# Optimization experiments

Hardware: AMD Instinct MI355X
Metric: run time of the kernel (lower is better)

The kernel has to match this reference:

```python
import jax, jax.numpy as jnp
import numpy as np
from jax import lax

RADIUS = 5


def setup_inputs() -> dict:
    key = jax.random.key(0)
    k1, k2 = jax.random.split(key)
    B, K, H, W = 4, 6, 128, 128
    win = 2 * RADIUS + 1
    labels = jax.random.uniform(k1, (B, K, H, W), dtype=jnp.float32)
    weights = jax.random.uniform(k2, (B, H * W, win, win), dtype=jnp.float32)
    return {"labels": labels, "weights": weights}


def reference(labels, weights):
    # labels:  [B, K, H, W]  class probabilities
    B, K, H, W = labels.shape
    win = 2 * RADIUS + 1
    N = H * W

    # Extract 11x11 patches around every pixel for all classes at once.
    patches = lax.conv_general_dilated_patches(
        labels, (win, win), (1, 1), padding=[(RADIUS, RADIUS), (RADIUS, RADIUS)]
    )
    patches = patches.reshape(B, K, win * win, N)

    w = weights.reshape(B, N, win * win)

    # sum over window of weights * P, per class: wp[b,k,n] = sum_o w[b,n,o] * patches[b,k,o,n]
    wp = jnp.einsum('bkon,bno->bkn', patches, w)

    p = labels.reshape(B, K, N)
    num = jnp.einsum('bkn,bkn->bk', p, wp)          # association
    den = jnp.einsum('bkn,bn->bk', p, w.sum(-1))    # degree
    L = num / den                                    # [B, K]

    # nn.L1Loss()(L, zeros) per class = mean_b |L[b,k]|
    losses = jnp.mean(jnp.abs(L), axis=0)            # [K]
    return K - jnp.sum(losses)
```

## Files before the change

### kernel.cpp

```cpp
#include <hip/hip_runtime.h>

#define RADIUS 5
#define WIN    11
#define WIN2   121
#define KCLS   6
#define HH     128
#define WW     128
#define BB     4
#define NPIX   (HH*WW)
#define TPB    128
#define PXB    32
#define NBLK   (BB*HH*(WW/PXB))
#define LABW   (PXB + 2*RADIUS)
#define NSITE  (WIN*LABW)
#define PLSTR  (NSITE*2)

__global__ __launch_bounds__(TPB, 4) void ncut_main(
    const float* __restrict__ labels,
    const float* __restrict__ weights,
    float* __restrict__ part) {
  __shared__ float shl[3 * PLSTR];
  __shared__ float shred[2 * 12];

  const int tid = threadIdx.x;
  const int blk = blockIdx.x;
  const int b   = blk >> 9;
  const int rem = blk & 511;
  const int y0  = rem >> 2;
  const int x0  = (rem & 3) * PXB;

  const float* labB = labels + (size_t)b * KCLS * NPIX;
  for (int s = tid; s < NSITE; s += TPB) {
    const int tr = s / LABW;
    const int tc = s - tr * LABW;
    const int gy = y0 - RADIUS + tr;
    const int gx = x0 + tc - RADIUS;
    const bool ok = ((unsigned)gy < (unsigned)HH) & ((unsigned)gx < (unsigned)WW);
    const float* lp = labB + (size_t)gy * WW + gx;
#pragma unroll
    for (int p = 0; p < 3; ++p) {
      float2 v = make_float2(0.f, 0.f);
      if (ok) {
        v.x = lp[(size_t)(2 * p) * NPIX];
        v.y = lp[(size_t)(2 * p + 1) * NPIX];
      }
      *reinterpret_cast<float2*>(shl + p * PLSTR + 2 * s) = v;
    }
  }
  __syncthreads();

  const int px = tid >> 2;
  const int q  = tid & 3;
  const size_t pxg = (size_t)b * NPIX + (size_t)y0 * WW + x0 + px;
  const int S  = (int)(pxg & 3);
  const float* wal = weights + pxg * WIN2 - S;
  const int T0 = 4 * q - S;

  float2 a0 = make_float2(0.f, 0.f);
  float2 a1 = make_float2(0.f, 0.f);
  float2 a2 = make_float2(0.f, 0.f);
  float wsum = 0.f;

#pragma unroll
  for (int g = 0; g < 8; ++g) {
    const int kq = (g == 7) ? ((q == 3) ? 30 : 28 + q) : 4 * g + q;
    const float4 wv = *reinterpret_cast<const float4*>(wal + 4 * kq);
#pragma unroll
    for (int m = 0; m < 4; ++m) {
      float w = (m == 0) ? wv.x : (m == 1) ? wv.y : (m == 2) ? wv.z : wv.w;
      int   t = 16 * g + m + T0;
      bool valid = true;
      if (g == 0) valid = (q != 0) | (m >= S);
      if (g == 7) valid = (q < 2) | ((q == 2) & (m <= S));
      if (!valid) { w = 0.0f; t = 0; }
      const int r  = (t * 5958) >> 16;
      const int li = px + t + (LABW - WIN) * r;
      const float2 v0 = *reinterpret_cast<const float2*>(shl + 2 * li);
      const float2 v1 = *reinterpret_cast<const float2*>(shl + PLSTR + 2 * li);
      const float2 v2 = *reinterpret_cast<const float2*>(shl + 2 * PLSTR + 2 * li);
      wsum += w;
      a0.x += w * v0.x; a0.y += w * v0.y;
      a1.x += w * v1.x; a1.y += w * v1.y;
      a2.x += w * v2.x; a2.y += w * v2.y;
    }
  }

#pragma unroll
  for (int off = 1; off <= 2; off <<= 1) {
    wsum += __shfl_xor(wsum, off);
    a0.x += __shfl_xor(a0.x, off); a0.y += __shfl_xor(a0.y, off);
    a1.x += __shfl_xor(a1.x, off); a1.y += __shfl_xor(a1.y, off);
    a2.x += __shfl_xor(a2.x, off); a2.y += __shfl_xor(a2.y, off);
  }

  const int lc = px + 5 * LABW + 5;
  const float2 c0 = *reinterpret_cast<const float2*>(shl + 2 * lc);
  const float2 c1 = *reinterpret_cast<const float2*>(shl + PLSTR + 2 * lc);
  const float2 c2 = *reinterpret_cast<const float2*>(shl + 2 * PLSTR + 2 * lc);
  float nv[KCLS] = {c0.x * a0.x, c0.y * a0.y, c1.x * a1.x,
                    c1.y * a1.y, c2.x * a2.x, c2.y * a2.y};
  float dv[KCLS] = {c0.x * wsum, c0.y * wsum, c1.x * wsum,
                    c1.y * wsum, c2.x * wsum, c2.y * wsum};

#pragma unroll
  for (int off = 4; off <= 32; off <<= 1) {
#pragma unroll
    for (int k = 0; k < KCLS; ++k) {
      nv[k] += __shfl_xor(nv[k], off);
      dv[k] += __shfl_xor(dv[k], off);
    }
  }
  const int wave = tid >> 6;
  if ((tid & 63) == 0) {
#pragma unroll
    for (int k = 0; k < KCLS; ++k) {
      shred[wave * 12 + k]     = nv[k];
      shred[wave * 12 + 6 + k] = dv[k];
    }
  }
  __syncthreads();
  if (tid < 12) {
    part[tid * NBLK + blk] = shred[tid] + shred[12 + tid];
  }
}

__global__ __launch_bounds__(256) void ncut_final(
    const float* __restrict__ part, float* __restrict__ out) {
  __shared__ float shf[4 * 48];
  const int t     = threadIdx.x;
  const int sumid = t >> 2;
  const int seg   = t & 3;
  if (sumid < 48) {
    const int isden = sumid / 24;
    const int bk    = sumid - isden * 24;
    const int b     = bk / KCLS;
    const int k     = bk - b * KCLS;
    const int slot  = isden * KCLS + k;
    const float* p  = part + (size_t)slot * NBLK + b * (NBLK / BB) + seg * 128;
    float s = 0.f;
#pragma unroll 8
    for (int i = 0; i < 32; ++i) {
      const float4 v = *reinterpret_cast<const float4*>(p + 4 * i);
      s += v.x + v.y + v.z + v.w;
    }
    shf[seg * 48 + sumid] = s;
  }
  __syncthreads();
  float val = 0.f;
  if (t < 24) {
    float num = 0.f, den = 0.f;
#pragma unroll
    for (int sg = 0; sg < 4; ++sg) {
      num += shf[sg * 48 + t];
      den += shf[sg * 48 + 24 + t];
    }
    val = fabsf(num / den) * (1.0f / BB);
  }
  if (t < 64) {
#pragma unroll
    for (int off = 32; off; off >>= 1) val += __shfl_down(val, off);
    if (t == 0) out[0] = (float)KCLS - val;
  }
}

extern "C" void kernel_launch(void* const* d_in, const int* in_sizes, int n_in,
                              void* d_out, int out_size, void* d_ws, size_t ws_size,
                              hipStream_t stream) {
  const float* labels  = (const float*)d_in[0];
  const float* weights = (const float*)d_in[1];
  float* out  = (float*)d_out;
  float* part = (float*)d_ws;

  ncut_main<<<NBLK, TPB, 0, stream>>>(labels, weights, part);
  ncut_final<<<1, 256, 0, stream>>>(part, out);
}
```

Measured before the change: 19.04 us.

## Fuse final reduction into main kernel via last-block atomic counter

Result: slower. 53.16 us (+179.1%).

```diff
diff --git a/kernel.cpp b/kernel.cpp
--- a/kernel.cpp
+++ b/kernel.cpp
@@ -15,12 +15,15 @@
 #define NSITE  (WIN*LABW)
 #define PLSTR  (NSITE*2)
 
-__global__ __launch_bounds__(TPB, 4) void ncut_main(
+__global__ __launch_bounds__(TPB, 4) void ncut_fused(
     const float* __restrict__ labels,
     const float* __restrict__ weights,
-    float* __restrict__ part) {
+    float* __restrict__ part,
+    unsigned* __restrict__ counter,
+    float* __restrict__ out) {
   __shared__ float shl[3 * PLSTR];
   __shared__ float shred[2 * 12];
+  __shared__ int   lastFlag;
 
   const int tid = threadIdx.x;
   const int blk = blockIdx.x;
@@ -119,48 +122,44 @@
     }
   }
   __syncthreads();
+
   if (tid < 12) {
-    part[tid * NBLK + blk] = shred[tid] + shred[12 + tid];
+    const float s = shred[tid] + shred[12 + tid];
+    __hip_atomic_store(part + tid * NBLK + blk, s,
+                       __ATOMIC_RELAXED, __HIP_MEMORY_SCOPE_AGENT);
   }
-}
+  __syncthreads();
+  if (tid == 0) {
+    unsigned old = __hip_atomic_fetch_add(counter, 1u, __ATOMIC_RELAXED,
+                                          __HIP_MEMORY_SCOPE_AGENT);
+    lastFlag = (old == NBLK - 1) ? 1 : 0;
+  }
+  __syncthreads();
+  if (!lastFlag) return;
 
-__global__ __launch_bounds__(256) void ncut_final(
-    const float* __restrict__ part, float* __restrict__ out) {
-  __shared__ float shf[4 * 48];
-  const int t     = threadIdx.x;
-  const int sumid = t >> 2;
-  const int seg   = t & 3;
+  float s = 0.f;
+  const int sumid = tid >> 1;
   if (sumid < 48) {
     const int isden = sumid / 24;
     const int bk    = sumid - isden * 24;
-    const int b     = bk / KCLS;
-    const int k     = bk - b * KCLS;
-    const int slot  = isden * KCLS + k;
-    const float* p  = part + (size_t)slot * NBLK + b * (NBLK / BB) + seg * 128;
-    float s = 0.f;
+    const int fb    = bk / KCLS;
+    const int fk    = bk - fb * KCLS;
+    const int slot  = isden * KCLS + fk;
+    const float* p  = part + (size_t)slot * NBLK + fb * (NBLK / BB)
+                      + (tid & 1) * 256;
 #pragma unroll 8
-    for (int i = 0; i < 32; ++i) {
-      const float4 v = *reinterpret_cast<const float4*>(p + 4 * i);
-      s += v.x + v.y + v.z + v.w;
-    }
-    shf[seg * 48 + sumid] = s;
+    for (int i = 0; i < 256; ++i)
+      s += __hip_atomic_load(p + i, __ATOMIC_RELAXED,
+                             __HIP_MEMORY_SCOPE_AGENT);
   }
+  s += __shfl_xor(s, 1);
+  if (((tid & 1) == 0) && sumid < 48) shl[sumid] = s;
   __syncthreads();
   float val = 0.f;
-  if (t < 24) {
-    float num = 0.f, den = 0.f;
+  if (tid < 24) val = fabsf(shl[tid] / shl[24 + tid]) * (1.0f / BB);
 #pragma unroll
-    for (int sg = 0; sg < 4; ++sg) {
-      num += shf[sg * 48 + t];
-      den += shf[sg * 48 + 24 + t];
-    }
-    val = fabsf(num / den) * (1.0f / BB);
-  }
-  if (t < 64) {
-#pragma unroll
-    for (int off = 32; off; off >>= 1) val += __shfl_down(val, off);
-    if (t == 0) out[0] = (float)KCLS - val;
-  }
+  for (int off = 32; off; off >>= 1) val += __shfl_down(val, off);
+  if (tid == 0) out[0] = (float)KCLS - val;
 }
 
 extern "C" void kernel_launch(void* const* d_in, const int* in_sizes, int n_in,
@@ -168,9 +167,10 @@
                               hipStream_t stream) {
   const float* labels  = (const float*)d_in[0];
   const float* weights = (const float*)d_in[1];
-  float* out  = (float*)d_out;
-  float* part = (float*)d_ws;
+  float* out = (float*)d_out;
+  float*    part    = (float*)d_ws;
+  unsigned* counter = (unsigned*)((char*)d_ws + 12 * NBLK * 4);
 
-  ncut_main<<<NBLK, TPB, 0, stream>>>(labels, weights, part);
-  ncut_final<<<1, 256, 0, stream>>>(part, out);
+  hipMemsetAsync(counter, 0, 4, stream);
+  ncut_fused<<<NBLK, TPB, 0, stream>>>(labels, weights, part, counter, out);
 }
```
